# Optimization experiments

Measured on AMD Instinct MI355X. Metric: run time of the kernel, lower is better.

The kernel has to match this reference:

```python
import jax, jax.numpy as jnp
import numpy as np
from jax import lax

B, C, HW = 8, 512, 32
NH = 8            # num_heads
NG = 32           # num_groups
HD = C // NH      # head_size = 64
EPS = 1e-6


def group_norm(x, gamma, beta, groups=NG, eps=EPS):
    b, c, h, w = x.shape
    xr = x.reshape(b, groups, c // groups, h, w)
    mu = xr.mean(axis=(2, 3, 4), keepdims=True)
    var = xr.var(axis=(2, 3, 4), keepdims=True)
    xn = ((xr - mu) / jnp.sqrt(var + eps)).reshape(b, c, h, w)
    return xn * gamma[None, :, None, None] + beta[None, :, None, None]


def conv2d(x, w, b):
    y = lax.conv_general_dilated(x, w, (1, 1), 'SAME',
                                 dimension_numbers=('NCHW', 'OIHW', 'NCHW'))
    return y + b[None, :, None, None]


def setup_inputs() -> dict:
    key = jax.random.key(0)
    ks = jax.random.split(key, 24)
    f32 = jnp.float32

    def lin(k, out_d, in_d):
        return (jax.random.normal(k, (out_d, in_d), f32) / np.sqrt(in_d)).astype(f32)

    inp = {
        'hidden_states': jax.random.normal(ks[0], (B, C, HW, HW), f32),
        'pre_g': jnp.ones(C, f32), 'pre_b': jnp.zeros(C, f32),
        'norm_g': jnp.ones(C, f32), 'norm_b': jnp.zeros(C, f32),
        'post_g': jnp.ones(C, f32), 'post_b': jnp.zeros(C, f32),
        'pos_emb': jax.random.normal(ks[1], (1, C, 32, 32), f32) * 0.02,
        'sa_w1': (jax.random.normal(ks[2], (C // 8, C, 1, 1), f32) / np.sqrt(C)),
        'sa_b1': jnp.zeros(C // 8, f32),
        'sa_w2': (jax.random.normal(ks[3], (C // 8, C // 8, 3, 3), f32) / np.sqrt(9 * C // 8)),
        'sa_b2': jnp.zeros(C // 8, f32),
        'sa_w3': (jax.random.normal(ks[4], (1, C // 8, 1, 1), f32) / np.sqrt(C // 8)),
        'sa_b3': jnp.zeros(1, f32),
        'wq': lin(ks[5], C, C), 'wk': lin(ks[6], C, C), 'wv': lin(ks[7], C, C),
        'wq0': lin(ks[8], C // 2, C), 'wk0': lin(ks[9], C // 2, C), 'wv0': lin(ks[10], C // 2, C),
        'wq1': lin(ks[11], C // 2, C), 'wk1': lin(ks[12], C // 2, C), 'wv1': lin(ks[13], C // 2, C),
        'ff_w1': lin(ks[14], C, 2 * C), 'ff_b1': jnp.zeros(C, f32),
        'ff_w2': lin(ks[15], C, C), 'ff_b2': jnp.zeros(C, f32),
        'out_w': lin(ks[16], C, C), 'out_b': jnp.zeros(C, f32),
    }
    return inp


def reference(hidden_states, pre_g, pre_b, norm_g, norm_b, post_g, post_b,
              pos_emb, sa_w1, sa_b1, sa_w2, sa_b2, sa_w3, sa_b3,
              wq, wk, wv, wq0, wk0, wv0, wq1, wk1, wv1,
              ff_w1, ff_b1, ff_w2, ff_b2, out_w, out_b):
    b, c, h, w = hidden_states.shape
    S = h * w
    residual = hidden_states

    hs = group_norm(hidden_states, pre_g, pre_b)
    # H=W=32 matches pos_embedding; bilinear resize to same size is identity
    hs = hs + pos_emb

    # spatial attention gating (conv 1x1 -> SiLU -> conv 3x3 -> SiLU -> conv 1x1 -> sigmoid)
    a = jax.nn.silu(conv2d(hs, sa_w1, sa_b1))
    a = jax.nn.silu(conv2d(a, sa_w2, sa_b2))
    spatial_weights = jax.nn.sigmoid(conv2d(a, sa_w3, sa_b3))
    spatial_enhanced = hs * spatial_weights

    # standard multi-head self-attention over flattened tokens
    sh = group_norm(hs, norm_g, norm_b).reshape(b, c, S).transpose(0, 2, 1)  # (B,S,C)
    ehs = sh  # encoder_hidden_states defaults to standard_hidden

    q = (sh @ wq.T).reshape(b, S, NH, HD)
    k = (ehs @ wk.T).reshape(b, S, NH, HD)
    v = (ehs @ wv.T).reshape(b, S, NH, HD)
    scores = jnp.einsum('bqhd,bkhd->bhqk', q, k) / np.sqrt(HD)
    probs = jax.nn.softmax(scores, axis=-1)
    std_out = jnp.einsum('bhqk,bkhd->bqhd', probs, v).reshape(b, S, c)

    # two multi-scale single-head attention branches (dim C/2 each)
    msh = spatial_enhanced.reshape(b, c, S).transpose(0, 2, 1)  # (B,S,C)
    parts = []
    for wqm, wkm, wvm in ((wq0, wk0, wv0), (wq1, wk1, wv1)):
        qm = msh @ wqm.T          # (B,S,C/2)
        km = ehs @ wkm.T
        vm = ehs @ wvm.T
        sc = jnp.einsum('bqd,bkd->bqk', qm, km) / np.sqrt(c // 2)
        parts.append(jnp.einsum('bqk,bkd->bqd', jax.nn.softmax(sc, axis=-1), vm))
    multi_out = jnp.concatenate(parts, axis=-1)  # (B,S,C)

    combined = jnp.concatenate([std_out, multi_out], axis=-1)  # (B,S,2C)
    fused = jax.nn.silu(combined @ ff_w1.T + ff_b1) @ ff_w2.T + ff_b2  # dropout = eval identity
    final = fused @ out_w.T + out_b
    final = final.transpose(0, 2, 1).reshape(b, c, h, w)
    final = group_norm(final, post_g, post_b)
    return final + residual
```

## Files before the change

### kernel.cpp

```cpp
#include <hip/hip_runtime.h>
#include <hip/hip_bf16.h>
#include <math.h>

typedef __attribute__((ext_vector_type(8))) __bf16 v8bf;
typedef __attribute__((ext_vector_type(4))) float v4f;

__device__ __forceinline__ unsigned short f2bf(float f) {
  union { float f; unsigned int u; } a; a.f = f;
  unsigned int r = a.u + 0x7fffu + ((a.u >> 16) & 1u);
  return (unsigned short)(r >> 16);
}
__device__ __forceinline__ unsigned short f2bf_trunc(float f) {
  union { float f; unsigned int u; } a; a.f = f;
  return (unsigned short)(a.u >> 16);
}
__device__ __forceinline__ float bf2f(unsigned short u) {
  union { unsigned int i; float f; } a; a.i = ((unsigned int)u) << 16; return a.f;
}
__device__ __forceinline__ float sigm(float x) { return 1.0f / (1.0f + __expf(-x)); }

__device__ __forceinline__ void async16(const void* g, void* l) {
  __builtin_amdgcn_global_load_lds(
      (const __attribute__((address_space(1))) unsigned int*)g,
      (__attribute__((address_space(3))) unsigned int*)l, 16, 0, 0);
}

__global__ __launch_bounds__(256) void gn_pre_kernel(
    const float* __restrict__ x, const float* __restrict__ g, const float* __restrict__ be,
    const float* __restrict__ pos, unsigned short* __restrict__ hsb, float* __restrict__ stats) {
  __shared__ float L[16384];
  __shared__ float rs[4], rs2[4], mr[2];
  int b = blockIdx.x >> 5, grp = blockIdx.x & 31;
  const float4* base = (const float4*)(x + ((size_t)b*512 + grp*16)*1024);
  float4* L4 = (float4*)L;
  int w = threadIdx.x >> 6;
  float s = 0.f, s2 = 0.f;
  for (int i = threadIdx.x; i < 4096; i += 256) {
    float4 v = base[i];
    L4[i] = v;
    s += v.x + v.y + v.z + v.w;
    s2 += v.x*v.x + v.y*v.y + v.z*v.z + v.w*v.w;
  }
#pragma unroll
  for (int o = 32; o; o >>= 1) { s += __shfl_xor(s, o); s2 += __shfl_xor(s2, o); }
  if ((threadIdx.x & 63) == 0) { rs[w] = s; rs2[w] = s2; }
  __syncthreads();
  if (threadIdx.x == 0) {
    float ts = rs[0]+rs[1]+rs[2]+rs[3], ts2 = rs2[0]+rs2[1]+rs2[2]+rs2[3];
    float mu = ts * (1.0f/16384.0f);
    float var = ts2 * (1.0f/16384.0f) - mu*mu;
    mr[0] = mu; mr[1] = rsqrtf(var + 1e-6f);
  }
  __syncthreads();
  float mu = mr[0], rstd = mr[1];
  const float4* pb = (const float4*)(pos + (size_t)grp*16*1024);
  float ns = 0.f, ns2 = 0.f;
  for (int i = threadIdx.x; i < 4096; i += 256) {
    float4 v = L4[i], p = pb[i];
    int c = grp*16 + (i >> 8);
    float gg = g[c], bb = be[c];
    float4 o;
    o.x = (v.x - mu)*rstd*gg + bb + p.x;
    o.y = (v.y - mu)*rstd*gg + bb + p.y;
    o.z = (v.z - mu)*rstd*gg + bb + p.z;
    o.w = (v.w - mu)*rstd*gg + bb + p.w;
    L4[i] = o;
    ns += o.x + o.y + o.z + o.w;
    ns2 += o.x*o.x + o.y*o.y + o.z*o.z + o.w*o.w;
  }
#pragma unroll
  for (int o = 32; o; o >>= 1) { ns += __shfl_xor(ns, o); ns2 += __shfl_xor(ns2, o); }
  if ((threadIdx.x & 63) == 0) { rs[w] = ns; rs2[w] = ns2; }
  __syncthreads();
  if (threadIdx.x == 0) {
    float ts = rs[0]+rs[1]+rs[2]+rs[3], ts2 = rs2[0]+rs2[1]+rs2[2]+rs2[3];
    float nmu = ts * (1.0f/16384.0f);
    float nvar = ts2 * (1.0f/16384.0f) - nmu*nmu;
    stats[(b*32+grp)*2] = nmu; stats[(b*32+grp)*2+1] = rsqrtf(nvar + 1e-6f);
  }
#pragma unroll
  for (int j = 0; j < 4; ++j) {
    int sI = threadIdx.x + j*256;
    unsigned int wd[8];
#pragma unroll
    for (int c = 0; c < 8; ++c) {
      unsigned int lo = f2bf(L[(2*c)*1024 + sI]);
      unsigned int hi = f2bf(L[(2*c+1)*1024 + sI]);
      wd[c] = lo | (hi << 16);
    }
    size_t oo = (size_t)(b*1024 + sI)*512 + grp*16;
    *(uint4*)(hsb + oo)     = make_uint4(wd[0], wd[1], wd[2], wd[3]);
    *(uint4*)(hsb + oo + 8) = make_uint4(wd[4], wd[5], wd[6], wd[7]);
  }
}

__global__ __launch_bounds__(256) void im2col_kernel(
    const unsigned short* __restrict__ a1, unsigned short* __restrict__ im2) {
  int row0 = blockIdx.x * 8;
#pragma unroll
  for (int it = 0; it < 3; ++it) {
    int cc = it*256 + threadIdx.x;
    if (cc >= 576) break;
    int rl = cc / 72, rr = cc - rl*72;
    int tap = rr >> 3, ch8 = rr & 7;
    int row = row0 + rl;
    int bb = row >> 10, s = row & 1023;
    int y = s >> 5, xx0 = s & 31;
    int yy = y + tap/3 - 1, xx = xx0 + tap%3 - 1;
    ushort4 v0 = make_ushort4(0,0,0,0), v1 = make_ushort4(0,0,0,0);
    if ((unsigned)yy < 32u && (unsigned)xx < 32u) {
      const unsigned short* src = a1 + ((size_t)(bb*1024 + yy*32 + xx))*64 + ch8*8;
      v0 = *(const ushort4*)src; v1 = *(const ushort4*)(src + 4);
    }
    unsigned short* dst = im2 + (size_t)row*576 + tap*64 + ch8*8;
    *(ushort4*)dst = v0; *(ushort4*)(dst + 4) = v1;
  }
}

__global__ __launch_bounds__(256) void gate_norm_kernel(
    const unsigned short* __restrict__ hsb, const unsigned short* __restrict__ a2,
    const float* __restrict__ w3, const float* __restrict__ b3,
    const float* __restrict__ stats, const float* __restrict__ g,
    const float* __restrict__ be,
    unsigned short* __restrict__ sh, unsigned short* __restrict__ msh) {
  int b = blockIdx.y;
  int s = blockIdx.x * 4 + (threadIdx.x >> 6);
  int oct = threadIdx.x & 63;
  int c0 = oct * 8;
  int grp = c0 >> 4;
  float part = bf2f(a2[((size_t)(b*1024) + s)*64 + oct]) * w3[oct];
#pragma unroll
  for (int o = 32; o; o >>= 1) part += __shfl_xor(part, o);
  float wgt = sigm(part + b3[0]);
  float mu = stats[(b*32 + grp)*2], rstd = stats[(b*32 + grp)*2 + 1];
  size_t o = (size_t)(b*1024 + s)*512 + c0;
  ushort4 u0 = *(const ushort4*)(hsb + o), u1 = *(const ushort4*)(hsb + o + 4);
  unsigned short uu[8] = {u0.x,u0.y,u0.z,u0.w,u1.x,u1.y,u1.z,u1.w};
  unsigned short so[8], mo[8];
#pragma unroll
  for (int j = 0; j < 8; ++j) {
    float v = bf2f(uu[j]);
    so[j] = f2bf((v - mu)*rstd*g[c0+j] + be[c0+j]);
    mo[j] = f2bf(v * wgt);
  }
  *(ushort4*)(sh + o)     = make_ushort4(so[0], so[1], so[2], so[3]);
  *(ushort4*)(sh + o + 4) = make_ushort4(so[4], so[5], so[6], so[7]);
  *(ushort4*)(msh + o)     = make_ushort4(mo[0], mo[1], mo[2], mo[3]);
  *(ushort4*)(msh + o + 4) = make_ushort4(mo[4], mo[5], mo[6], mo[7]);
}

struct WCvt { const float* src; int dstOff; int n; float scale; };
struct WCvtArgs { WCvt w[15]; };
__global__ __launch_bounds__(256) void wconvert_kernel(WCvtArgs a, unsigned short* __restrict__ dst) {
  WCvt e = a.w[blockIdx.y];
  int i = blockIdx.x * 256 + threadIdx.x;
  if (i >= e.n) return;
  if (blockIdx.y == 13) {
    int oc = i / 576, r = i - oc*576;
    int tap = r >> 6, ic = r & 63;
    dst[e.dstOff + i] = f2bf(e.src[(oc*64 + ic)*9 + tap]);
  } else if (blockIdx.y == 14) {
    dst[e.dstOff + i] = f2bf(e.src[(i & 511)*512 + (i >> 9)]);
  } else {
    dst[e.dstOff + i] = f2bf(e.src[i] * e.scale);
  }
}

__global__ __launch_bounds__(256) void bias_fold_kernel(
    const float* __restrict__ ow, const float* __restrict__ b2,
    const float* __restrict__ ob, float* __restrict__ bc) {
  int n = blockIdx.x * 256 + threadIdx.x;
  float s = ob[n];
  const float* r = ow + (size_t)n * 512;
#pragma unroll 8
  for (int j = 0; j < 512; ++j) s += r[j] * b2[j];
  bc[n] = s;
}

__global__ __launch_bounds__(256) void transpose2_kernel(
    const unsigned short* __restrict__ qkvm,
    unsigned short* __restrict__ vtb, unsigned short* __restrict__ vmt) {
  __shared__ unsigned short t[64][65];
  int s0 = blockIdx.x * 64, c0 = blockIdx.y * 64;
  int z = blockIdx.z, b = z & 7;
  const unsigned short* in = qkvm + (z >= 8 ? 2048 : 1024);
  unsigned short* out = (z >= 8) ? vmt : vtb;
  int tx = threadIdx.x & 63, ty = threadIdx.x >> 6;
#pragma unroll
  for (int i = 0; i < 16; ++i) {
    int s = ty + i*4;
    t[s][tx] = in[((size_t)(b*1024 + s0 + s))*2560 + c0 + tx];
  }
  __syncthreads();
#pragma unroll
  for (int i = 0; i < 16; ++i) {
    int c = ty + i*4;
    out[((size_t)b*512 + c0 + c)*1024 + s0 + tx] = t[tx][c];
  }
}

struct GemmDesc {
  const unsigned short* A; const unsigned short* B; void* out; const float* bias;
  int M, N, K, lda, ldb, ldo, epi;
  long long Ay, Az, By, Bz, Oy, Oz;
};

template<int BM, int BN>
__global__ __launch_bounds__(256) void gemm_tile_kernel(GemmDesc d) {
  constexpr int WGM = (BN >= 128) ? 2 : 4;
  constexpr int WGN = 4 / WGM;
  constexpr int MT = BM / (16 * WGM);
  constexpr int NT = BN / (16 * WGN);
  constexpr int AIT = (BM * 8) / 256;
  constexpr int BIT = (BN * 8) / 256;
  __shared__ __align__(16) unsigned short As[BM * 64];
  __shared__ __align__(16) unsigned short Bs[BN * 64];

  int ntx = d.N / BN, mtx = d.M / BM;
  int bmt, bnt;
  if ((mtx & 7) == 0) {
    int xcd = blockIdx.x & 7, j = blockIdx.x >> 3;
    int mpx = mtx >> 3;
    bmt = xcd * mpx + (j % mpx);
    bnt = j / mpx;
  } else {
    bmt = blockIdx.x / ntx; bnt = blockIdx.x % ntx;
  }
  int bm0 = bmt * BM, bn0 = bnt * BN;
  const unsigned short* A = d.A + (long long)blockIdx.y * d.Ay
      + (long long)blockIdx.z * d.Az + (size_t)bm0 * d.lda;
  const unsigned short* B = d.B + (long long)blockIdx.y * d.By
      + (long long)blockIdx.z * d.Bz + (size_t)bn0 * d.ldb;
  int tid = threadIdx.x, lane = tid & 63, w = tid >> 6;
  int wm = (WGN == 2) ? (w >> 1) : w;
  int wn = (WGN == 2) ? (w & 1) : 0;
  int ln = lane & 15, qd = lane >> 4;

  v4f acc[MT][NT];
#pragma unroll
  for (int i = 0; i < MT; ++i)
#pragma unroll
    for (int j = 0; j < NT; ++j) acc[i][j] = (v4f){0.f, 0.f, 0.f, 0.f};

  int nks = d.K >> 6;
  for (int ks = 0; ks < nks; ++ks) {
    int kof = ks * 64;
#pragma unroll
    for (int it = 0; it < AIT; ++it) {
      int c = it * 256 + tid;
      int row = c >> 3, ch = c & 7;
      async16(A + (size_t)row * d.lda + ((ch ^ (row & 7)) << 3) + kof, As + c * 8);
    }
#pragma unroll
    for (int it = 0; it < BIT; ++it) {
      int c = it * 256 + tid;
      int row = c >> 3, ch = c & 7;
      async16(B + (size_t)row * d.ldb + ((ch ^ (row & 7)) << 3) + kof, Bs + c * 8);
    }
    __syncthreads();
#pragma unroll
    for (int k2 = 0; k2 < 2; ++k2) {
      v8bf af[MT], bfr[NT];
#pragma unroll
      for (int i = 0; i < MT; ++i) {
        int row = wm * MT * 16 + i * 16 + ln;
        af[i] = *(const v8bf*)(As + row * 64 + (((k2*4 + qd) ^ (ln & 7)) << 3));
      }
#pragma unroll
      for (int j = 0; j < NT; ++j) {
        int row = wn * NT * 16 + j * 16 + ln;
        bfr[j] = *(const v8bf*)(Bs + row * 64 + (((k2*4 + qd) ^ (ln & 7)) << 3));
      }
#pragma unroll
      for (int i = 0; i < MT; ++i)
#pragma unroll
        for (int j = 0; j < NT; ++j)
          acc[i][j] = __builtin_amdgcn_mfma_f32_16x16x32_bf16(af[i], bfr[j], acc[i][j], 0, 0, 0);
    }
    __syncthreads();
  }

  size_t obase = (size_t)((long long)blockIdx.y * d.Oy + (long long)blockIdx.z * d.Oz);
#pragma unroll
  for (int i = 0; i < MT; ++i) {
#pragma unroll
    for (int j = 0; j < NT; ++j) {
      int col = bn0 + wn * NT * 16 + j * 16 + ln;
      float bia = d.bias ? d.bias[col] : 0.0f;
#pragma unroll
      for (int r = 0; r < 4; ++r) {
        int row = bm0 + wm * MT * 16 + i * 16 + qd * 4 + r;
        float v = acc[i][j][r] + bia;
        if (d.epi == 2) v = v * sigm(v);
        size_t oi = obase + (size_t)row * d.ldo + col;
        if (d.epi == 0) ((float*)d.out)[oi] = v;
        else ((unsigned short*)d.out)[oi] = f2bf(v);
      }
    }
  }
}

__global__ __launch_bounds__(512) void flash_attn_kernel(
    const unsigned short* __restrict__ QKVM, const unsigned short* __restrict__ VTB,
    unsigned short* __restrict__ out) {
  __shared__ __align__(16) unsigned short Ks[128*64];
  __shared__ __align__(16) unsigned short Vts[64*128];
  __shared__ __align__(16) unsigned short Pw[8][16*128];
  int h = blockIdx.x, b = blockIdx.y, qt = blockIdx.z;
  int tid = threadIdx.x, lane = tid & 63, w = tid >> 6;
  int ln = lane & 15, qd = lane >> 4;

  const unsigned short* Qbase = QKVM + ((size_t)(b*1024 + qt*128 + w*16))*2560 + h*64;
  v8bf aq[2];
#pragma unroll
  for (int s = 0; s < 2; ++s)
    aq[s] = *(const v8bf*)(Qbase + (size_t)ln*2560 + s*32 + qd*8);

  v4f o_acc[4];
  float l_part[4];
#pragma unroll
  for (int dn = 0; dn < 4; ++dn) o_acc[dn] = (v4f){0.f,0.f,0.f,0.f};
#pragma unroll
  for (int r = 0; r < 4; ++r) l_part[r] = 0.f;

  const unsigned short* Kg = QKVM + 512 + (size_t)(b*1024)*2560 + h*64;
  const unsigned short* Vg = VTB + ((size_t)(b*512) + h*64)*1024;

  for (int kt = 0; kt < 8; ++kt) {
#pragma unroll
    for (int it = 0; it < 2; ++it) {
      int c = it*512 + tid;
      async16(Kg + (size_t)(kt*128 + (c >> 3))*2560 + (((c & 7) ^ ((c >> 3) & 7)) << 3),
              Ks + c*8);
    }
#pragma unroll
    for (int it = 0; it < 2; ++it) {
      int c = it*512 + tid;
      async16(Vg + (size_t)(c >> 4)*1024 + kt*128 + ((((c & 15) ^ ((c >> 4) & 7))) << 3),
              Vts + c*8);
    }
    __syncthreads();

    v4f sc[8];
#pragma unroll
    for (int n = 0; n < 8; ++n) {
      v4f a = (v4f){0.f,0.f,0.f,0.f};
#pragma unroll
      for (int s = 0; s < 2; ++s) {
        v8bf kb = *(const v8bf*)(Ks + (n*16 + ln)*64 + (((s*4 + qd) ^ (ln & 7)) << 3));
        a = __builtin_amdgcn_mfma_f32_16x16x32_bf16(aq[s], kb, a, 0, 0, 0);
      }
      sc[n] = a;
    }
#pragma unroll
    for (int r = 0; r < 4; ++r) {
      int row7 = (qd*4 + r) & 7;
      float acc_l = 0.f;
#pragma unroll
      for (int n = 0; n < 8; ++n) {
        float p = exp2f(sc[n][r]);
        acc_l += p;
        Pw[w][(qd*4 + r)*128 + (((n*2 + (ln >> 3)) ^ row7) << 3) + (ln & 7)] = f2bf_trunc(p);
      }
      l_part[r] += acc_l;
    }
#pragma unroll
    for (int dn = 0; dn < 4; ++dn) {
      v4f a = o_acc[dn];
#pragma unroll
      for (int ks2 = 0; ks2 < 4; ++ks2) {
        int phys = (((ks2*4 + qd) ^ (ln & 7)) << 3);
        v8bf pf = *(const v8bf*)(&Pw[w][ln*128 + phys]);
        v8bf vf = *(const v8bf*)(Vts + (dn*16 + ln)*128 + phys);
        a = __builtin_amdgcn_mfma_f32_16x16x32_bf16(pf, vf, a, 0, 0, 0);
      }
      o_acc[dn] = a;
    }
    __syncthreads();
  }

  unsigned short* ob = out + ((size_t)(b*1024 + qt*128 + w*16))*1024 + h*64;
#pragma unroll
  for (int r = 0; r < 4; ++r) {
    float l = l_part[r];
    l += __shfl_xor(l, 1); l += __shfl_xor(l, 2);
    l += __shfl_xor(l, 4); l += __shfl_xor(l, 8);
    float rinv = 1.0f / l;
#pragma unroll
    for (int dn = 0; dn < 4; ++dn)
      ob[(size_t)(qd*4 + r)*1024 + dn*16 + ln] = f2bf(o_acc[dn][r] * rinv);
  }
}

__global__ __launch_bounds__(256) void flash_branch_kernel(
    const unsigned short* __restrict__ QKVM, const unsigned short* __restrict__ QM,
    const unsigned short* __restrict__ VMT, float* __restrict__ OP, float* __restrict__ LP) {
  __shared__ __align__(16) unsigned short Ks[64*256];
  __shared__ __align__(16) unsigned short Vts[256*64];
  __shared__ __align__(16) unsigned short Pw[4][16*64];
  int bb = blockIdx.x, b = bb >> 1, br = bb & 1;
  int kh = blockIdx.y, qt = blockIdx.z;
  int tid = threadIdx.x, lane = tid & 63, w = tid >> 6;
  int ln = lane & 15, qd = lane >> 4;

  const unsigned short* Qb = QM + ((size_t)(b*1024 + qt*64 + w*16))*512 + br*256;
  v8bf aq[8];
#pragma unroll
  for (int s = 0; s < 8; ++s)
    aq[s] = *(const v8bf*)(Qb + (size_t)ln*512 + s*32 + qd*8);

  v4f o_acc[16];
  float l_part[4];
#pragma unroll
  for (int dn = 0; dn < 16; ++dn) o_acc[dn] = (v4f){0.f,0.f,0.f,0.f};
#pragma unroll
  for (int r = 0; r < 4; ++r) l_part[r] = 0.f;

  const unsigned short* Kg = QKVM + 1536 + br*256 + (size_t)(b*1024)*2560;
  const unsigned short* Vg = VMT + ((size_t)(b*512) + br*256)*1024;

  for (int kt = kh*8; kt < kh*8 + 8; ++kt) {
#pragma unroll
    for (int it = 0; it < 8; ++it) {
      int c = it*256 + tid;
      int row = c >> 5, ch = c & 31;
      async16(Kg + (size_t)(kt*64 + row)*2560 + ((ch ^ (row & 7)) << 3), Ks + c*8);
    }
#pragma unroll
    for (int it = 0; it < 8; ++it) {
      int c = it*256 + tid;
      int row = c >> 3, ch = c & 7;
      async16(Vg + (size_t)row*1024 + kt*64 + ((ch ^ (row & 7)) << 3), Vts + c*8);
    }
    __syncthreads();

    v4f sc[4];
#pragma unroll
    for (int n = 0; n < 4; ++n) {
      v4f a = (v4f){0.f,0.f,0.f,0.f};
      int krow = n*16 + ln;
#pragma unroll
      for (int s = 0; s < 8; ++s) {
        v8bf kb = *(const v8bf*)(Ks + krow*256 + (((s*4 + qd) ^ (krow & 7)) << 3));
        a = __builtin_amdgcn_mfma_f32_16x16x32_bf16(aq[s], kb, a, 0, 0, 0);
      }
      sc[n] = a;
    }
#pragma unroll
    for (int r = 0; r < 4; ++r) {
      int row7 = (qd*4 + r) & 7;
      float acc_l = 0.f;
#pragma unroll
      for (int n = 0; n < 4; ++n) {
        float p = exp2f(sc[n][r]);
        acc_l += p;
        Pw[w][(qd*4 + r)*64 + (((n*2 + (ln >> 3)) ^ row7) << 3) + (ln & 7)] = f2bf_trunc(p);
      }
      l_part[r] += acc_l;
    }
#pragma unroll
    for (int dn = 0; dn < 16; ++dn) {
      v4f a = o_acc[dn];
#pragma unroll
      for (int ks2 = 0; ks2 < 2; ++ks2) {
        int phys = (((ks2*4 + qd) ^ (ln & 7)) << 3);
        v8bf pf = *(const v8bf*)(&Pw[w][ln*64 + phys]);
        v8bf vf = *(const v8bf*)(Vts + (dn*16 + ln)*64 + phys);
        a = __builtin_amdgcn_mfma_f32_16x16x32_bf16(pf, vf, a, 0, 0, 0);
      }
      o_acc[dn] = a;
    }
    __syncthreads();
  }

  int slot = ((bb*16 + qt)*2 + kh);
  float* Ob = OP + (size_t)slot*16384;
  float* Lb = LP + (size_t)slot*64;
#pragma unroll
  for (int r = 0; r < 4; ++r) {
    int row = w*16 + qd*4 + r;
    float l = l_part[r];
    l += __shfl_xor(l, 1); l += __shfl_xor(l, 2);
    l += __shfl_xor(l, 4); l += __shfl_xor(l, 8);
    if (ln == 0) Lb[row] = l;
#pragma unroll
    for (int dn = 0; dn < 16; ++dn)
      Ob[(size_t)row*256 + dn*16 + ln] = o_acc[dn][r];
  }
}

__global__ __launch_bounds__(256) void branch_combine_kernel(
    const float* __restrict__ OP, const float* __restrict__ LP,
    unsigned short* __restrict__ out) {
  int bb = blockIdx.x, qt = blockIdx.y;
  int b = bb >> 1, br = bb & 1;
  int slot0 = (bb*16 + qt)*2, slot1 = slot0 + 1;
  int row = threadIdx.x >> 2, cseg = (threadIdx.x & 3) * 64;
  float l = LP[(size_t)slot0*64 + row] + LP[(size_t)slot1*64 + row];
  float rinv = 1.0f / l;
  const float4* o0 = (const float4*)(OP + (size_t)slot0*16384 + (size_t)row*256 + cseg);
  const float4* o1 = (const float4*)(OP + (size_t)slot1*16384 + (size_t)row*256 + cseg);
  unsigned short* ob = out + ((size_t)(b*1024 + qt*64 + row))*1024 + 512 + br*256 + cseg;
#pragma unroll
  for (int i = 0; i < 16; ++i) {
    float4 a = o0[i], c = o1[i];
    ob[i*4+0] = f2bf((a.x + c.x) * rinv);
    ob[i*4+1] = f2bf((a.y + c.y) * rinv);
    ob[i*4+2] = f2bf((a.z + c.z) * rinv);
    ob[i*4+3] = f2bf((a.w + c.w) * rinv);
  }
}

__global__ __launch_bounds__(256) void gn_stats_bf16_kernel(
    const unsigned short* __restrict__ t, float* __restrict__ stats) {
  int b = blockIdx.x >> 5, grp = blockIdx.x & 31;
  float s = 0.f, s2 = 0.f;
#pragma unroll
  for (int j = 0; j < 4; ++j) {
    int sI = threadIdx.x + j*256;
    const unsigned short* p = t + ((size_t)(b*1024 + sI))*512 + grp*16;
    uint4 a = *(const uint4*)p, c2 = *(const uint4*)(p + 8);
    unsigned int ww[8] = {a.x,a.y,a.z,a.w,c2.x,c2.y,c2.z,c2.w};
#pragma unroll
    for (int k = 0; k < 8; ++k) {
      float lo = bf2f((unsigned short)(ww[k] & 0xffff));
      float hi = bf2f((unsigned short)(ww[k] >> 16));
      s += lo + hi; s2 += lo*lo + hi*hi;
    }
  }
#pragma unroll
  for (int o = 32; o; o >>= 1) { s += __shfl_xor(s, o); s2 += __shfl_xor(s2, o); }
  __shared__ float rs[4], rs2[4];
  int w = threadIdx.x >> 6;
  if ((threadIdx.x & 63) == 0) { rs[w] = s; rs2[w] = s2; }
  __syncthreads();
  if (threadIdx.x == 0) {
    float ts = rs[0]+rs[1]+rs[2]+rs[3], ts2 = rs2[0]+rs2[1]+rs2[2]+rs2[3];
    float mu = ts * (1.0f/16384.0f);
    float var = ts2 * (1.0f/16384.0f) - mu*mu;
    stats[(b*32+grp)*2] = mu; stats[(b*32+grp)*2+1] = rsqrtf(var + 1e-6f);
  }
}

__global__ __launch_bounds__(256) void final_out_kernel(
    const unsigned short* __restrict__ fin, const float* __restrict__ stats,
    const float* __restrict__ g, const float* __restrict__ be,
    const float* __restrict__ x, float* __restrict__ out) {
  __shared__ float t[64][65];
  int s0 = blockIdx.x * 64, c0 = blockIdx.y * 64, b = blockIdx.z;
  int tx = threadIdx.x & 63, ty = threadIdx.x >> 6;
#pragma unroll
  for (int i = 0; i < 16; ++i) {
    int s = ty + i*4;
    t[s][tx] = bf2f(fin[((size_t)(b*1024 + s0 + s))*512 + c0 + tx]);
  }
  __syncthreads();
#pragma unroll
  for (int i = 0; i < 16; ++i) {
    int c = ty + i*4;
    int cc = c0 + c, grp = cc >> 4;
    float mu = stats[(b*32+grp)*2], rstd = stats[(b*32+grp)*2+1];
    float gg = g[cc], bb = be[cc];
    size_t oi = ((size_t)(b*512 + cc))*1024 + s0 + tx;
    out[oi] = (t[tx][c] - mu)*rstd*gg + bb + x[oi];
  }
}

static void launch_gemm128(hipStream_t st, const unsigned short* A, const unsigned short* B,
                           void* out, const float* bias,
                           int M, int N, int K, int lda, int ldb, int ldo, int epi,
                           long long Ay, long long Az, long long By, long long Bz,
                           long long Oy, long long Oz, int gy, int gz) {
  GemmDesc d{A, B, out, bias, M, N, K, lda, ldb, ldo, epi, Ay, Az, By, Bz, Oy, Oz};
  gemm_tile_kernel<128,128><<<dim3((M/128)*(N/128), gy, gz), dim3(256), 0, st>>>(d);
}
static void launch_gemm64(hipStream_t st, const unsigned short* A, const unsigned short* B,
                          void* out, const float* bias,
                          int M, int N, int K, int lda, int ldb, int ldo, int epi) {
  GemmDesc d{A, B, out, bias, M, N, K, lda, ldb, ldo, epi, 0,0,0,0,0,0};
  gemm_tile_kernel<128,64><<<dim3((M/128)*(N/64), 1, 1), dim3(256), 0, st>>>(d);
}

extern "C" void kernel_launch(void* const* d_in, const int* in_sizes, int n_in,
                              void* d_out, int out_size, void* d_ws, size_t ws_size,
                              hipStream_t stream) {
  const float* x      = (const float*)d_in[0];
  const float* pre_g  = (const float*)d_in[1];
  const float* pre_b  = (const float*)d_in[2];
  const float* norm_g = (const float*)d_in[3];
  const float* norm_b = (const float*)d_in[4];
  const float* post_g = (const float*)d_in[5];
  const float* post_b = (const float*)d_in[6];
  const float* pos    = (const float*)d_in[7];
  const float* sa_b1  = (const float*)d_in[9];
  const float* sa_b2  = (const float*)d_in[11];
  const float* sa_w3  = (const float*)d_in[12];
  const float* sa_b3  = (const float*)d_in[13];
  const float* ff_b1  = (const float*)d_in[24];
  const float* ff_b2  = (const float*)d_in[26];
  const float* out_w  = (const float*)d_in[27];
  const float* out_b  = (const float*)d_in[28];
  float* outp = (float*)d_out;

  char* ws = (char*)d_ws;
  size_t off = 0;
  auto alloc = [&](size_t bytes) -> void* {
    void* p = ws + off; off += (bytes + 255) & ~(size_t)255; return p;
  };
  float* STATS = (float*)alloc(4096);
  float* BC    = (float*)alloc(2048);
  unsigned short* HSB  = (unsigned short*)alloc(8388608);
  unsigned short* A1   = (unsigned short*)alloc(1048576);
  unsigned short* IM2  = (unsigned short*)alloc(9437184);
  unsigned short* A2   = (unsigned short*)alloc(1048576);
  unsigned short* SHB  = (unsigned short*)alloc(8388608);
  unsigned short* MSHB = (unsigned short*)alloc(8388608);
  unsigned short* WBF  = (unsigned short*)alloc(6291456);
  unsigned short* WCOMB= (unsigned short*)alloc(524288);
  unsigned short* QKVM = (unsigned short*)alloc(41943040);
  unsigned short* QM   = (unsigned short*)alloc(8388608);
  unsigned short* VTB  = (unsigned short*)alloc(8388608);
  unsigned short* VMT  = (unsigned short*)alloc(8388608);
  unsigned short* COMB = (unsigned short*)alloc(16777216);
  unsigned short* FFMID= (unsigned short*)alloc(8388608);
  unsigned short* FINALB=(unsigned short*)alloc(8388608);
  float* OP    = (float*)alloc(33554432);
  float* LP    = (float*)alloc(131072);

  const int OQKVM=0, OQM=1310720, OFF1=1572864, OFF2T=2097152,
            OOW=2359296, OW1=2621440, OW2R=2654208;

  gn_pre_kernel<<<dim3(256), dim3(256), 0, stream>>>(x, pre_g, pre_b, pos, HSB, STATS);
  {
    WCvtArgs a;
    const float LG2E = 1.4426950408889634f;
    const int   srcIdx[15] = {14,15,16, 18,21,19,22, 17,20, 23,27, 8, 0, 10, 25};
    const int   dofs[15]   = {0, 262144, 524288,
                              786432, 917504, 1048576, 1179648,
                              OQM, OQM+131072,
                              OFF1, OOW, OW1, 0, OW2R, OFF2T};
    const int   ns[15]     = {262144,262144,262144, 131072,131072,131072,131072,
                              131072,131072, 524288,262144, 32768, 0, 36864, 262144};
    const float sc[15]     = {0.125f*LG2E,1.f,1.f, 1.f,1.f,1.f,1.f,
                              0.0625f*LG2E,0.0625f*LG2E, 1.f,1.f, 1.f, 0.f, 1.f, 1.f};
    for (int i = 0; i < 15; ++i) { a.w[i].src = (const float*)d_in[srcIdx[i]]; a.w[i].dstOff = dofs[i]; a.w[i].n = ns[i]; a.w[i].scale = sc[i]; }
    wconvert_kernel<<<dim3(2048, 15), dim3(256), 0, stream>>>(a, WBF);
  }
  {
    GemmDesc d{WBF+OOW, WBF+OFF2T, WCOMB, nullptr, 512, 512, 512, 512, 512, 512, 1, 0,0,0,0,0,0};
    gemm_tile_kernel<128,128><<<dim3(16, 1, 1), dim3(256), 0, stream>>>(d);
  }
  bias_fold_kernel<<<dim3(2), dim3(256), 0, stream>>>(out_w, ff_b2, out_b, BC);
  launch_gemm64(stream, HSB, WBF+OW1,  A1, sa_b1, 8192, 64, 512, 512, 512, 64, 2);
  im2col_kernel<<<dim3(1024), dim3(256), 0, stream>>>(A1, IM2);
  launch_gemm64(stream, IM2, WBF+OW2R, A2, sa_b2, 8192, 64, 576, 576, 576, 64, 2);
  gate_norm_kernel<<<dim3(256, 8), dim3(256), 0, stream>>>(HSB, A2, sa_w3, sa_b3, STATS, norm_g, norm_b, SHB, MSHB);

  launch_gemm128(stream, SHB,  WBF+OQKVM, QKVM, nullptr, 8192, 2560, 512, 512, 512, 2560, 1, 0,0,0,0,0,0, 1,1);
  launch_gemm64(stream, MSHB, WBF+OQM,   QM,   nullptr, 8192, 512,  512, 512, 512, 512,  1);

  transpose2_kernel<<<dim3(16, 8, 16), dim3(256), 0, stream>>>(QKVM, VTB, VMT);

  flash_attn_kernel<<<dim3(8, 8, 8), dim3(512), 0, stream>>>(QKVM, VTB, COMB);

  flash_branch_kernel<<<dim3(16, 2, 16), dim3(256), 0, stream>>>(QKVM, QM, VMT, OP, LP);
  branch_combine_kernel<<<dim3(16, 16), dim3(256), 0, stream>>>(OP, LP, COMB);

  launch_gemm64(stream, COMB,  WBF+OFF1, FFMID,  ff_b1, 8192, 512, 1024, 1024, 1024, 512, 2);
  launch_gemm64(stream, FFMID, WCOMB,    FINALB, BC,    8192, 512, 512,  512,  512,  512, 1);

  gn_stats_bf16_kernel<<<dim3(256), dim3(256), 0, stream>>>(FINALB, STATS);
  final_out_kernel<<<dim3(16, 8, 8), dim3(256), 0, stream>>>(FINALB, STATS, post_g, post_b, x, outp);

  (void)in_sizes; (void)n_in; (void)out_size; (void)ws_size;
}
```

Before: 402.0 us.

## Process two 16-row query subtiles per wave in attention kernels

Both flash attention kernels now give each wave 32 query rows, split into two 16-row MFMA subtiles. Each K and V fragment read from LDS is reused for both subtiles, and the grids and the combine kernel are resized to match. The aim is to halve K/V global and LDS traffic per query and to amortise the barriers. In exchange the grid has half as many blocks and each thread holds more accumulator registers, which may reduce occupancy or cause spills.

Measured after the change: 400.5 us. Within noise of the previous version (-0.4%).

```diff
diff --git a/kernel.cpp b/kernel.cpp
--- a/kernel.cpp
+++ b/kernel.cpp
@@ -305,23 +305,28 @@
     unsigned short* __restrict__ out) {
   __shared__ __align__(16) unsigned short Ks[128*64];
   __shared__ __align__(16) unsigned short Vts[64*128];
-  __shared__ __align__(16) unsigned short Pw[8][16*128];
+  __shared__ __align__(16) unsigned short Pw[8][32*128];
   int h = blockIdx.x, b = blockIdx.y, qt = blockIdx.z;
   int tid = threadIdx.x, lane = tid & 63, w = tid >> 6;
   int ln = lane & 15, qd = lane >> 4;
 
-  const unsigned short* Qbase = QKVM + ((size_t)(b*1024 + qt*128 + w*16))*2560 + h*64;
-  v8bf aq[2];
-#pragma unroll
-  for (int s = 0; s < 2; ++s)
-    aq[s] = *(const v8bf*)(Qbase + (size_t)ln*2560 + s*32 + qd*8);
-
-  v4f o_acc[4];
-  float l_part[4];
-#pragma unroll
-  for (int dn = 0; dn < 4; ++dn) o_acc[dn] = (v4f){0.f,0.f,0.f,0.f};
-#pragma unroll
-  for (int r = 0; r < 4; ++r) l_part[r] = 0.f;
+  const unsigned short* Qbase = QKVM + ((size_t)(b*1024 + qt*256 + w*32))*2560 + h*64;
+  v8bf aq[2][2];
+#pragma unroll
+  for (int i = 0; i < 2; ++i)
+#pragma unroll
+    for (int s = 0; s < 2; ++s)
+      aq[i][s] = *(const v8bf*)(Qbase + (size_t)(i*16 + ln)*2560 + s*32 + qd*8);
+
+  v4f o_acc[2][4];
+  float l_part[2][4];
+#pragma unroll
+  for (int i = 0; i < 2; ++i) {
+#pragma unroll
+    for (int dn = 0; dn < 4; ++dn) o_acc[i][dn] = (v4f){0.f,0.f,0.f,0.f};
+#pragma unroll
+    for (int r = 0; r < 4; ++r) l_part[i][r] = 0.f;
+  }
 
   const unsigned short* Kg = QKVM + 512 + (size_t)(b*1024)*2560 + h*64;
   const unsigned short* Vg = VTB + ((size_t)(b*512) + h*64)*1024;
@@ -341,55 +346,65 @@
     }
     __syncthreads();
 
-    v4f sc[8];
-#pragma unroll
-    for (int n = 0; n < 8; ++n) {
-      v4f a = (v4f){0.f,0.f,0.f,0.f};
+    v4f sc[2][8];
+#pragma unroll
+    for (int i = 0; i < 2; ++i)
+#pragma unroll
+      for (int n = 0; n < 8; ++n) sc[i][n] = (v4f){0.f,0.f,0.f,0.f};
+#pragma unroll
+    for (int n = 0; n < 8; ++n)
 #pragma unroll
       for (int s = 0; s < 2; ++s) {
         v8bf kb = *(const v8bf*)(Ks + (n*16 + ln)*64 + (((s*4 + qd) ^ (ln & 7)) << 3));
-        a = __builtin_amdgcn_mfma_f32_16x16x32_bf16(aq[s], kb, a, 0, 0, 0);
-      }
-      sc[n] = a;
-    }
+#pragma unroll
+        for (int i = 0; i < 2; ++i)
+          sc[i][n] = __builtin_amdgcn_mfma_f32_16x16x32_bf16(aq[i][s], kb, sc[i][n], 0, 0, 0);
+      }
+#pragma unroll
+    for (int i = 0; i < 2; ++i)
+#pragma unroll
+      for (int r = 0; r < 4; ++r) {
+        int row7 = (qd*4 + r) & 7;
+        float acc_l = 0.f;
+#pragma unroll
+        for (int n = 0; n < 8; ++n) {
+          float p = exp2f(sc[i][n][r]);
+          acc_l += p;
+          Pw[w][(i*16 + qd*4 + r)*128 + (((n*2 + (ln >> 3)) ^ row7) << 3) + (ln & 7)] = f2bf_trunc(p);
+        }
+        l_part[i][r] += acc_l;
+      }
+    v8bf pf[2][4];
+#pragma unroll
+    for (int i = 0; i < 2; ++i)
+#pragma unroll
+      for (int ks2 = 0; ks2 < 4; ++ks2)
+        pf[i][ks2] = *(const v8bf*)(&Pw[w][(i*16 + ln)*128 + (((ks2*4 + qd) ^ (ln & 7)) << 3)]);
+#pragma unroll
+    for (int dn = 0; dn < 4; ++dn)
+#pragma unroll
+      for (int ks2 = 0; ks2 < 4; ++ks2) {
+        v8bf vf = *(const v8bf*)(Vts + (dn*16 + ln)*128 + (((ks2*4 + qd) ^ (ln & 7)) << 3));
+#pragma unroll
+        for (int i = 0; i < 2; ++i)
+          o_acc[i][dn] = __builtin_amdgcn_mfma_f32_16x16x32_bf16(pf[i][ks2], vf, o_acc[i][dn], 0, 0, 0);
+      }
+    __syncthreads();
+  }
+
+  unsigned short* ob = out + ((size_t)(b*1024 + qt*256 + w*32))*1024 + h*64;
+#pragma unroll
+  for (int i = 0; i < 2; ++i)
 #pragma unroll
     for (int r = 0; r < 4; ++r) {
-      int row7 = (qd*4 + r) & 7;
-      float acc_l = 0.f;
-#pragma unroll
-      for (int n = 0; n < 8; ++n) {
-        float p = exp2f(sc[n][r]);
-        acc_l += p;
-        Pw[w][(qd*4 + r)*128 + (((n*2 + (ln >> 3)) ^ row7) << 3) + (ln & 7)] = f2bf_trunc(p);
-      }
-      l_part[r] += acc_l;
-    }
-#pragma unroll
-    for (int dn = 0; dn < 4; ++dn) {
-      v4f a = o_acc[dn];
-#pragma unroll
-      for (int ks2 = 0; ks2 < 4; ++ks2) {
-        int phys = (((ks2*4 + qd) ^ (ln & 7)) << 3);
-        v8bf pf = *(const v8bf*)(&Pw[w][ln*128 + phys]);
-        v8bf vf = *(const v8bf*)(Vts + (dn*16 + ln)*128 + phys);
-        a = __builtin_amdgcn_mfma_f32_16x16x32_bf16(pf, vf, a, 0, 0, 0);
-      }
-      o_acc[dn] = a;
-    }
-    __syncthreads();
-  }
-
-  unsigned short* ob = out + ((size_t)(b*1024 + qt*128 + w*16))*1024 + h*64;
-#pragma unroll
-  for (int r = 0; r < 4; ++r) {
-    float l = l_part[r];
-    l += __shfl_xor(l, 1); l += __shfl_xor(l, 2);
-    l += __shfl_xor(l, 4); l += __shfl_xor(l, 8);
-    float rinv = 1.0f / l;
-#pragma unroll
-    for (int dn = 0; dn < 4; ++dn)
-      ob[(size_t)(qd*4 + r)*1024 + dn*16 + ln] = f2bf(o_acc[dn][r] * rinv);
-  }
+      float l = l_part[i][r];
+      l += __shfl_xor(l, 1); l += __shfl_xor(l, 2);
+      l += __shfl_xor(l, 4); l += __shfl_xor(l, 8);
+      float rinv = 1.0f / l;
+#pragma unroll
+      for (int dn = 0; dn < 4; ++dn)
+        ob[(size_t)(i*16 + qd*4 + r)*1024 + dn*16 + ln] = f2bf(o_acc[i][dn][r] * rinv);
+    }
 }
 
 __global__ __launch_bounds__(256) void flash_branch_kernel(
@@ -397,24 +412,29 @@
     const unsigned short* __restrict__ VMT, float* __restrict__ OP, float* __restrict__ LP) {
   __shared__ __align__(16) unsigned short Ks[64*256];
   __shared__ __align__(16) unsigned short Vts[256*64];
-  __shared__ __align__(16) unsigned short Pw[4][16*64];
+  __shared__ __align__(16) unsigned short Pw[4][32*64];
   int bb = blockIdx.x, b = bb >> 1, br = bb & 1;
   int kh = blockIdx.y, qt = blockIdx.z;
   int tid = threadIdx.x, lane = tid & 63, w = tid >> 6;
   int ln = lane & 15, qd = lane >> 4;
 
-  const unsigned short* Qb = QM + ((size_t)(b*1024 + qt*64 + w*16))*512 + br*256;
-  v8bf aq[8];
-#pragma unroll
-  for (int s = 0; s < 8; ++s)
-    aq[s] = *(const v8bf*)(Qb + (size_t)ln*512 + s*32 + qd*8);
-
-  v4f o_acc[16];
-  float l_part[4];
-#pragma unroll
-  for (int dn = 0; dn < 16; ++dn) o_acc[dn] = (v4f){0.f,0.f,0.f,0.f};
-#pragma unroll
-  for (int r = 0; r < 4; ++r) l_part[r] = 0.f;
+  const unsigned short* Qb = QM + ((size_t)(b*1024 + qt*128 + w*32))*512 + br*256;
+  v8bf aq[2][8];
+#pragma unroll
+  for (int i = 0; i < 2; ++i)
+#pragma unroll
+    for (int s = 0; s < 8; ++s)
+      aq[i][s] = *(const v8bf*)(Qb + (size_t)(i*16 + ln)*512 + s*32 + qd*8);
+
+  v4f o_acc[2][16];
+  float l_part[2][4];
+#pragma unroll
+  for (int i = 0; i < 2; ++i) {
+#pragma unroll
+    for (int dn = 0; dn < 16; ++dn) o_acc[i][dn] = (v4f){0.f,0.f,0.f,0.f};
+#pragma unroll
+    for (int r = 0; r < 4; ++r) l_part[i][r] = 0.f;
+  }
 
   const unsigned short* Kg = QKVM + 1536 + br*256 + (size_t)(b*1024)*2560;
   const unsigned short* Vg = VMT + ((size_t)(b*512) + br*256)*1024;
@@ -434,59 +454,68 @@
     }
     __syncthreads();
 
-    v4f sc[4];
-#pragma unroll
-    for (int n = 0; n < 4; ++n) {
-      v4f a = (v4f){0.f,0.f,0.f,0.f};
-      int krow = n*16 + ln;
+    v4f sc[2][4];
+#pragma unroll
+    for (int i = 0; i < 2; ++i)
+#pragma unroll
+      for (int n = 0; n < 4; ++n) sc[i][n] = (v4f){0.f,0.f,0.f,0.f};
+#pragma unroll
+    for (int n = 0; n < 4; ++n)
 #pragma unroll
       for (int s = 0; s < 8; ++s) {
-        v8bf kb = *(const v8bf*)(Ks + krow*256 + (((s*4 + qd) ^ (krow & 7)) << 3));
-        a = __builtin_amdgcn_mfma_f32_16x16x32_bf16(aq[s], kb, a, 0, 0, 0);
-      }
-      sc[n] = a;
-    }
+        v8bf kb = *(const v8bf*)(Ks + (n*16 + ln)*256 + (((s*4 + qd) ^ (ln & 7)) << 3));
+#pragma unroll
+        for (int i = 0; i < 2; ++i)
+          sc[i][n] = __builtin_amdgcn_mfma_f32_16x16x32_bf16(aq[i][s], kb, sc[i][n], 0, 0, 0);
+      }
+#pragma unroll
+    for (int i = 0; i < 2; ++i)
+#pragma unroll
+      for (int r = 0; r < 4; ++r) {
+        int row7 = (qd*4 + r) & 7;
+        float acc_l = 0.f;
+#pragma unroll
+        for (int n = 0; n < 4; ++n) {
+          float p = exp2f(sc[i][n][r]);
+          acc_l += p;
+          Pw[w][(i*16 + qd*4 + r)*64 + (((n*2 + (ln >> 3)) ^ row7) << 3) + (ln & 7)] = f2bf_trunc(p);
+        }
+        l_part[i][r] += acc_l;
+      }
+    v8bf pf[2][2];
+#pragma unroll
+    for (int i = 0; i < 2; ++i)
+#pragma unroll
+      for (int ks2 = 0; ks2 < 2; ++ks2)
+        pf[i][ks2] = *(const v8bf*)(&Pw[w][(i*16 + ln)*64 + (((ks2*4 + qd) ^ (ln & 7)) << 3)]);
+#pragma unroll
+    for (int dn = 0; dn < 16; ++dn)
+#pragma unroll
+      for (int ks2 = 0; ks2 < 2; ++ks2) {
+        v8bf vf = *(const v8bf*)(Vts + (dn*16 + ln)*64 + (((ks2*4 + qd) ^ (ln & 7)) << 3));
+#pragma unroll
+        for (int i = 0; i < 2; ++i)
+          o_acc[i][dn] = __builtin_amdgcn_mfma_f32_16x16x32_bf16(pf[i][ks2], vf, o_acc[i][dn], 0, 0, 0);
+      }
+    __syncthreads();
+  }
+
+  int slot = ((bb*8 + qt)*2 + kh);
+  float* Ob = OP + (size_t)slot*32768;
+  float* Lb = LP + (size_t)slot*128;
+#pragma unroll
+  for (int i = 0; i < 2; ++i)
 #pragma unroll
     for (int r = 0; r < 4; ++r) {
-      int row7 = (qd*4 + r) & 7;
-      float acc_l = 0.f;
-#pragma unroll
-      for (int n = 0; n < 4; ++n) {
-        float p = exp2f(sc[n][r]);
-        acc_l += p;
-        Pw[w][(qd*4 + r)*64 + (((n*2 + (ln >> 3)) ^ row7) << 3) + (ln & 7)] = f2bf_trunc(p);
-      }
-      l_part[r] += acc_l;
-    }
-#pragma unroll
-    for (int dn = 0; dn < 16; ++dn) {
-      v4f a = o_acc[dn];
-#pragma unroll
-      for (int ks2 = 0; ks2 < 2; ++ks2) {
-        int phys = (((ks2*4 + qd) ^ (ln & 7)) << 3);
-        v8bf pf = *(const v8bf*)(&Pw[w][ln*64 + phys]);
-        v8bf vf = *(const v8bf*)(Vts + (dn*16 + ln)*64 + phys);
-        a = __builtin_amdgcn_mfma_f32_16x16x32_bf16(pf, vf, a, 0, 0, 0);
-      }
-      o_acc[dn] = a;
-    }
-    __syncthreads();
-  }
-
-  int slot = ((bb*16 + qt)*2 + kh);
-  float* Ob = OP + (size_t)slot*16384;
-  float* Lb = LP + (size_t)slot*64;
-#pragma unroll
-  for (int r = 0; r < 4; ++r) {
-    int row = w*16 + qd*4 + r;
-    float l = l_part[r];
-    l += __shfl_xor(l, 1); l += __shfl_xor(l, 2);
-    l += __shfl_xor(l, 4); l += __shfl_xor(l, 8);
-    if (ln == 0) Lb[row] = l;
-#pragma unroll
-    for (int dn = 0; dn < 16; ++dn)
-      Ob[(size_t)row*256 + dn*16 + ln] = o_acc[dn][r];
-  }
+      int row = w*32 + i*16 + qd*4 + r;
+      float l = l_part[i][r];
+      l += __shfl_xor(l, 1); l += __shfl_xor(l, 2);
+      l += __shfl_xor(l, 4); l += __shfl_xor(l, 8);
+      if (ln == 0) Lb[row] = l;
+#pragma unroll
+      for (int dn = 0; dn < 16; ++dn)
+        Ob[(size_t)row*256 + dn*16 + ln] = o_acc[i][dn][r];
+    }
 }
 
 __global__ __launch_bounds__(256) void branch_combine_kernel(
@@ -494,15 +523,15 @@
     unsigned short* __restrict__ out) {
   int bb = blockIdx.x, qt = blockIdx.y;
   int b = bb >> 1, br = bb & 1;
-  int slot0 = (bb*16 + qt)*2, slot1 = slot0 + 1;
-  int row = threadIdx.x >> 2, cseg = (threadIdx.x & 3) * 64;
-  float l = LP[(size_t)slot0*64 + row] + LP[(size_t)slot1*64 + row];
+  int slot0 = (bb*8 + qt)*2, slot1 = slot0 + 1;
+  int row = threadIdx.x >> 1, cseg = (threadIdx.x & 1) * 128;
+  float l = LP[(size_t)slot0*128 + row] + LP[(size_t)slot1*128 + row];
   float rinv = 1.0f / l;
-  const float4* o0 = (const float4*)(OP + (size_t)slot0*16384 + (size_t)row*256 + cseg);
-  const float4* o1 = (const float4*)(OP + (size_t)slot1*16384 + (size_t)row*256 + cseg);
-  unsigned short* ob = out + ((size_t)(b*1024 + qt*64 + row))*1024 + 512 + br*256 + cseg;
-#pragma unroll
-  for (int i = 0; i < 16; ++i) {
+  const float4* o0 = (const float4*)(OP + (size_t)slot0*32768 + (size_t)row*256 + cseg);
+  const float4* o1 = (const float4*)(OP + (size_t)slot1*32768 + (size_t)row*256 + cseg);
+  unsigned short* ob = out + ((size_t)(b*1024 + qt*128 + row))*1024 + 512 + br*256 + cseg;
+#pragma unroll
+  for (int i = 0; i < 32; ++i) {
     float4 a = o0[i], c = o1[i];
     ob[i*4+0] = f2bf((a.x + c.x) * rinv);
     ob[i*4+1] = f2bf((a.y + c.y) * rinv);
@@ -661,10 +690,10 @@
 
   transpose2_kernel<<<dim3(16, 8, 16), dim3(256), 0, stream>>>(QKVM, VTB, VMT);
 
-  flash_attn_kernel<<<dim3(8, 8, 8), dim3(512), 0, stream>>>(QKVM, VTB, COMB);
-
-  flash_branch_kernel<<<dim3(16, 2, 16), dim3(256), 0, stream>>>(QKVM, QM, VMT, OP, LP);
-  branch_combine_kernel<<<dim3(16, 16), dim3(256), 0, stream>>>(OP, LP, COMB);
+  flash_attn_kernel<<<dim3(8, 8, 4), dim3(512), 0, stream>>>(QKVM, VTB, COMB);
+
+  flash_branch_kernel<<<dim3(16, 2, 8), dim3(256), 0, stream>>>(QKVM, QM, VMT, OP, LP);
+  branch_combine_kernel<<<dim3(16, 8), dim3(256), 0, stream>>>(OP, LP, COMB);
 
   launch_gemm64(stream, COMB,  WBF+OFF1, FFMID,  ff_b1, 8192, 512, 1024, 1024, 1024, 512, 2);
   launch_gemm64(stream, FFMID, WCOMB,    FINALB, BC,    8192, 512, 512,  512,  512,  512, 1);
```
